# Performance work log

Measured on AMD Instinct MI355X. Metric: run time of the kernel, lower is better.

Reference implementation:

```python
import jax, jax.numpy as jnp
import numpy as np

N = 1024
IN_DIM = 64
H = 8
D = 8
E_REAL = 16384
GAMMA = 0.1


def setup_inputs() -> dict:
    key = jax.random.key(0)
    ks = jax.random.split(key, 12)
    inp = {
        "h": jax.random.normal(ks[0], (N, IN_DIM), dtype=jnp.float32),
        "e": jax.random.normal(ks[1], (E_REAL, IN_DIM), dtype=jnp.float32),
        "WQ": jax.random.normal(ks[2], (IN_DIM, H * D), dtype=jnp.float32) * 0.1,
        "WK": jax.random.normal(ks[3], (IN_DIM, H * D), dtype=jnp.float32) * 0.1,
        "WE": jax.random.normal(ks[4], (IN_DIM, H * D), dtype=jnp.float32) * 0.1,
        "WQ2": jax.random.normal(ks[5], (IN_DIM, H * D), dtype=jnp.float32) * 0.1,
        "WK2": jax.random.normal(ks[6], (IN_DIM, H * D), dtype=jnp.float32) * 0.1,
        "WE2": jax.random.normal(ks[7], (IN_DIM, H * D), dtype=jnp.float32) * 0.1,
        "WV": jax.random.normal(ks[8], (IN_DIM, H * D), dtype=jnp.float32) * 0.1,
        "real_src": jax.random.randint(ks[9], (E_REAL,), 0, N, dtype=jnp.int32),
        "real_dst": jax.random.randint(ks[10], (E_REAL,), 0, N, dtype=jnp.int32),
    }
    return inp


def reference(h, e, WQ, WK, WE, WQ2, WK2, WE2, WV, real_src, real_dst):
    scale = float(np.sqrt(D))
    # Dense edge-feature adjacency: adj[src, dst] = e  (zeros elsewhere)
    adj = jnp.zeros((N, N, IN_DIM), dtype=h.dtype).at[real_src, real_dst].set(e)
    # Edge projections over the dense adjacency (no bias): [N, N, H, D]
    Eh = (adj @ WE).reshape(N, N, H, D)
    E2h = (adj @ WE2).reshape(N, N, H, D)
    # Node projections: [N, H, D]
    Qh = (h @ WQ).reshape(N, H, D)
    Kh = (h @ WK).reshape(N, H, D)
    Q2h = (h @ WQ2).reshape(N, H, D)
    K2h = (h @ WK2).reshape(N, H, D)
    Vh = (h @ WV).reshape(N, H, D)
    # 3-way K*Q*E contraction over head dim: [N, N, H] (i = src, j = dst)
    weights_real = jnp.einsum('ihd,jhd,ijhd->ijh', Kh, Qh, Eh) / scale
    weights_fake = jnp.einsum('ihd,jhd,ijhd->ijh', K2h, Q2h, E2h) / scale
    weights_real_exp = jnp.exp(jnp.clip(weights_real, -5.0, 5.0)) / (GAMMA + 1.0)
    weights_fake_exp = GAMMA * jnp.exp(jnp.clip(weights_fake, -5.0, 5.0)) / (GAMMA + 1.0)
    # Blend: real-edge positions take the real attention value
    weights_final = weights_fake_exp.at[real_src, real_dst].set(
        weights_real_exp[real_src, real_dst])
    # Zero self-loops
    idx = jnp.arange(N)
    weights_final = weights_final.at[idx, idx].set(0.0)
    # Aggregate values at destination nodes: sum over src i -> [N, H, D]
    out = jnp.einsum('ijh,ihd->jhd', weights_final, Vh)
    # Normalizer: sum of attention weights per destination node [N, H, 1]
    z = jnp.sum(weights_final, axis=0).reshape(N, H, 1)
    return out / (z + 1e-6)
```

## Files before the change

### kernel.cpp

```cpp
#include <hip/hip_runtime.h>

#define NN     1024
#define INDIM  64
#define EREAL  16384
#define HD     64

__constant__ const float C_BASE    = 0.1f / 1.1f;
__constant__ const float INV_1P1   = 1.0f / 1.1f;
__constant__ const float INV_SCALE = 0.35355339059327373f;

__global__ void proj_kernel(const float* __restrict__ h,
                            const float* __restrict__ WQ,
                            const float* __restrict__ WK,
                            const float* __restrict__ WV,
                            float* __restrict__ Qh,
                            float* __restrict__ Kh,
                            float* __restrict__ Vh) {
    __shared__ float hrow[INDIM];
    const int row = blockIdx.x;
    const int t   = threadIdx.x;
    hrow[t] = h[row * INDIM + t];
    __syncthreads();
    float q = 0.f, k = 0.f, v = 0.f;
#pragma unroll 8
    for (int r = 0; r < INDIM; ++r) {
        const float hv = hrow[r];
        q += hv * WQ[r * HD + t];
        k += hv * WK[r * HD + t];
        v += hv * WV[r * HD + t];
    }
    Qh[row * HD + t] = q;
    Kh[row * HD + t] = k;
    Vh[row * HD + t] = v;
}

__global__ void colsum_kernel(const float* __restrict__ Vh, float* __restrict__ S) {
    __shared__ float part[4][HD];
    const int c = threadIdx.x & 63;
    const int p = threadIdx.x >> 6;
    float s = 0.f;
    for (int j = p * 256; j < p * 256 + 256; ++j) s += Vh[j * HD + c];
    part[p][c] = s;
    __syncthreads();
    if (p == 0) S[c] = part[0][c] + part[1][c] + part[2][c] + part[3][c];
}

__global__ void winner_kernel(const int* __restrict__ src, const int* __restrict__ dst,
                              int* __restrict__ winner) {
    const int k = blockIdx.x * 256 + threadIdx.x;
    if (k < EREAL) {
        const int key = src[k] * NN + dst[k];
        atomicMax(&winner[key], k + 1);
    }
}

__global__ void edge_kernel(const float* __restrict__ e,
                            const float* __restrict__ WE,
                            const float* __restrict__ Qh,
                            const float* __restrict__ Kh,
                            const float* __restrict__ Vh,
                            const int* __restrict__ src,
                            const int* __restrict__ dst,
                            const int* __restrict__ winner,
                            float* __restrict__ outacc,
                            float* __restrict__ zacc) {
    const int wid = threadIdx.x >> 6;
    const int k   = blockIdx.x * 4 + wid;
    const int t   = threadIdx.x & 63;
    const int s = src[k];
    const int d = dst[k];
    if (winner[s * NN + d] != k + 1 || s == d) return;

    const float ev = e[k * INDIM + t];
    float acc = 0.f;
#pragma unroll
    for (int r = 0; r < INDIM; ++r) {
        acc += __shfl(ev, r, 64) * WE[r * HD + t];
    }
    float term = Kh[s * HD + t] * Qh[d * HD + t] * acc;
    term += __shfl_xor(term, 1, 64);
    term += __shfl_xor(term, 2, 64);
    term += __shfl_xor(term, 4, 64);
    const float wr    = fminf(fmaxf(term * INV_SCALE, -5.f), 5.f);
    const float delta = expf(wr) * INV_1P1 - C_BASE;

    atomicAdd(&outacc[d * HD + t], delta * Vh[s * HD + t]);
    if ((t & 7) == 0) atomicAdd(&zacc[d * 8 + (t >> 3)], delta);
}

__global__ void finalize_kernel(const float* __restrict__ Vh,
                                const float* __restrict__ S,
                                const float* __restrict__ outacc,
                                const float* __restrict__ zacc,
                                float* __restrict__ out) {
    const int idx = blockIdx.x * 256 + threadIdx.x;
    const int j = idx >> 6;
    const int t = idx & 63;
    const float z = C_BASE * 1023.f + zacc[j * 8 + (t >> 3)] + 1e-6f;
    const float o = C_BASE * (S[t] - Vh[idx]) + outacc[idx];
    out[idx] = o / z;
}

extern "C" void kernel_launch(void* const* d_in, const int* in_sizes, int n_in,
                              void* d_out, int out_size, void* d_ws, size_t ws_size,
                              hipStream_t stream) {
    const float* h  = (const float*)d_in[0];
    const float* e  = (const float*)d_in[1];
    const float* WQ = (const float*)d_in[2];
    const float* WK = (const float*)d_in[3];
    const float* WE = (const float*)d_in[4];
    const float* WV = (const float*)d_in[8];
    const int* src  = (const int*)d_in[9];
    const int* dst  = (const int*)d_in[10];
    float* out = (float*)d_out;

    char* ws = (char*)d_ws;
    float* Qh = (float*)(ws + (0 << 10));
    float* Kh = (float*)(ws + (256 << 10));
    float* Vh = (float*)(ws + (512 << 10));
    float* S  = (float*)(ws + (768 << 10));
    char*  zreg   = ws + (1 << 20);
    float* outacc = (float*)zreg;
    float* zacc   = (float*)(zreg + (256 << 10));
    int*   winner = (int*)(zreg + (288 << 10));
    const size_t zbytes = (288 << 10) + (4u << 20);

    hipMemsetAsync(zreg, 0, zbytes, stream);
    hipLaunchKernelGGL(proj_kernel,    dim3(NN),   dim3(64),  0, stream, h, WQ, WK, WV, Qh, Kh, Vh);
    hipLaunchKernelGGL(colsum_kernel,  dim3(1),    dim3(256), 0, stream, Vh, S);
    hipLaunchKernelGGL(winner_kernel,  dim3(EREAL / 256), dim3(256), 0, stream, src, dst, winner);
    hipLaunchKernelGGL(edge_kernel,    dim3(EREAL / 4),   dim3(256), 0, stream,
                       e, WE, Qh, Kh, Vh, src, dst, winner, outacc, zacc);
    hipLaunchKernelGGL(finalize_kernel, dim3(NN * HD / 256), dim3(256), 0, stream,
                       Vh, S, outacc, zacc, out);
}
```

Measured before the change: 106.1 us.

## Fuse all stages into one cooperative kernel with grid syncs

Replaces the memset and five separate launches with a single cooperative kernel of 512 blocks. It runs projection, zeroing, winner resolution, column sums, edge processing and finalize as phases separated by grid.sync. The edge phase now has each wave handle 8 edges, broadcasting e values with readlane and reusing WE loads across them, and it uses the fast __expf. This removes launch gaps and the memset, at the cost of three grid-wide barriers and a fixed grid size tied to the problem dimensions.

Measured after the change: 279.2 us. +163.3%, slower.

```diff
diff --git a/kernel.cpp b/kernel.cpp
--- a/kernel.cpp
+++ b/kernel.cpp
@@ -1,104 +1,132 @@
 #include <hip/hip_runtime.h>
+#include <hip/hip_cooperative_groups.h>
+
+namespace cg = cooperative_groups;
 
 #define NN     1024
 #define INDIM  64
 #define EREAL  16384
 #define HD     64
+#define NBLK   512
+#define NTHR   256
 
-__constant__ const float C_BASE    = 0.1f / 1.1f;
-__constant__ const float INV_1P1   = 1.0f / 1.1f;
-__constant__ const float INV_SCALE = 0.35355339059327373f;
+constexpr float C_BASE    = 0.1f / 1.1f;
+constexpr float INV_1P1   = 1.0f / 1.1f;
+constexpr float INV_SCALE = 0.35355339059327373f;
 
-__global__ void proj_kernel(const float* __restrict__ h,
-                            const float* __restrict__ WQ,
-                            const float* __restrict__ WK,
-                            const float* __restrict__ WV,
-                            float* __restrict__ Qh,
-                            float* __restrict__ Kh,
-                            float* __restrict__ Vh) {
-    __shared__ float hrow[INDIM];
-    const int row = blockIdx.x;
-    const int t   = threadIdx.x;
-    hrow[t] = h[row * INDIM + t];
-    __syncthreads();
-    float q = 0.f, k = 0.f, v = 0.f;
-#pragma unroll 8
-    for (int r = 0; r < INDIM; ++r) {
-        const float hv = hrow[r];
-        q += hv * WQ[r * HD + t];
-        k += hv * WK[r * HD + t];
-        v += hv * WV[r * HD + t];
-    }
-    Qh[row * HD + t] = q;
-    Kh[row * HD + t] = k;
-    Vh[row * HD + t] = v;
+__device__ __forceinline__ float bcast(float v, int lane) {
+    return __uint_as_float(__builtin_amdgcn_readlane(__float_as_uint(v), lane));
 }
 
-__global__ void colsum_kernel(const float* __restrict__ Vh, float* __restrict__ S) {
-    __shared__ float part[4][HD];
-    const int c = threadIdx.x & 63;
-    const int p = threadIdx.x >> 6;
-    float s = 0.f;
-    for (int j = p * 256; j < p * 256 + 256; ++j) s += Vh[j * HD + c];
-    part[p][c] = s;
-    __syncthreads();
-    if (p == 0) S[c] = part[0][c] + part[1][c] + part[2][c] + part[3][c];
-}
+__global__ __launch_bounds__(NTHR, 2)
+void fused_kernel(const float* __restrict__ h,
+                  const float* __restrict__ e,
+                  const float* __restrict__ WQ,
+                  const float* __restrict__ WK,
+                  const float* __restrict__ WE,
+                  const float* __restrict__ WV,
+                  const int*   __restrict__ src,
+                  const int*   __restrict__ dst,
+                  float* __restrict__ Qh,
+                  float* __restrict__ Kh,
+                  float* __restrict__ Vh,
+                  float* __restrict__ outacc,
+                  float* __restrict__ zacc,
+                  float* __restrict__ Spart,
+                  int*   __restrict__ winner,
+                  float* __restrict__ out)
+{
+    cg::grid_group grid = cg::this_grid();
+    const int tid  = threadIdx.x;
+    const int bid  = blockIdx.x;
+    const int gtid = bid * NTHR + tid;
+    __shared__ float lds_buf[4][HD];
 
-__global__ void winner_kernel(const int* __restrict__ src, const int* __restrict__ dst,
-                              int* __restrict__ winner) {
-    const int k = blockIdx.x * 256 + threadIdx.x;
-    if (k < EREAL) {
-        const int key = src[k] * NN + dst[k];
-        atomicMax(&winner[key], k + 1);
+    if (bid >= 256) {
+        const int z = (bid - 256) * NTHR + tid;
+        const float4 zero4 = make_float4(0.f, 0.f, 0.f, 0.f);
+        float4* regA = (float4*)outacc;
+        if (z < 18688) regA[z] = zero4;
+        float4* regB = (float4*)winner;
+#pragma unroll
+        for (int i = 0; i < 4; ++i) regB[z + i * 65536] = zero4;
+    } else {
+        const int g = tid >> 6, c = tid & 63;
+        const int row = bid * 4 + g;
+        lds_buf[g][c] = h[row * INDIM + c];
+        __syncthreads();
+        float q = 0.f, k = 0.f, v = 0.f;
+#pragma unroll
+        for (int r = 0; r < INDIM; ++r) {
+            const float hv = lds_buf[g][r];
+            q = fmaf(hv, WQ[r * HD + c], q);
+            k = fmaf(hv, WK[r * HD + c], k);
+            v = fmaf(hv, WV[r * HD + c], v);
+        }
+        Qh[row * HD + c] = q;
+        Kh[row * HD + c] = k;
+        Vh[row * HD + c] = v;
     }
-}
+    grid.sync();
 
-__global__ void edge_kernel(const float* __restrict__ e,
-                            const float* __restrict__ WE,
-                            const float* __restrict__ Qh,
-                            const float* __restrict__ Kh,
-                            const float* __restrict__ Vh,
-                            const int* __restrict__ src,
-                            const int* __restrict__ dst,
-                            const int* __restrict__ winner,
-                            float* __restrict__ outacc,
-                            float* __restrict__ zacc) {
-    const int wid = threadIdx.x >> 6;
-    const int k   = blockIdx.x * 4 + wid;
-    const int t   = threadIdx.x & 63;
-    const int s = src[k];
-    const int d = dst[k];
-    if (winner[s * NN + d] != k + 1 || s == d) return;
+    if (gtid < EREAL) {
+        atomicMax(&winner[src[gtid] * NN + dst[gtid]], gtid + 1);
+    }
+    if (bid >= NBLK - 16) {
+        const int p = bid - (NBLK - 16);
+        const int g = tid >> 6, c = tid & 63;
+        float s = 0.f;
+        const int j0 = p * 64 + g * 16;
+        for (int j = j0; j < j0 + 16; ++j) s += Vh[j * HD + c];
+        lds_buf[g][c] = s;
+        __syncthreads();
+        if (g == 0)
+            Spart[p * HD + c] = lds_buf[0][c] + lds_buf[1][c] + lds_buf[2][c] + lds_buf[3][c];
+    }
+    grid.sync();
 
-    const float ev = e[k * INDIM + t];
-    float acc = 0.f;
+    {
+        const int wave = gtid >> 6;
+        const int t = tid & 63;
+        const int k0 = wave * 8;
+        float ev[8];
 #pragma unroll
-    for (int r = 0; r < INDIM; ++r) {
-        acc += __shfl(ev, r, 64) * WE[r * HD + t];
+        for (int i = 0; i < 8; ++i) ev[i] = e[(k0 + i) * INDIM + t];
+        float acc[8] = {0.f, 0.f, 0.f, 0.f, 0.f, 0.f, 0.f, 0.f};
+#pragma unroll
+        for (int r = 0; r < INDIM; ++r) {
+            const float w = WE[r * HD + t];
+#pragma unroll
+            for (int i = 0; i < 8; ++i)
+                acc[i] = fmaf(bcast(ev[i], r), w, acc[i]);
+        }
+#pragma unroll
+        for (int i = 0; i < 8; ++i) {
+            const int k = k0 + i;
+            const int s = src[k];
+            const int d = dst[k];
+            if (winner[s * NN + d] != k + 1 || s == d) continue;
+            float term = Kh[s * HD + t] * Qh[d * HD + t] * acc[i];
+            term += __shfl_xor(term, 1, 64);
+            term += __shfl_xor(term, 2, 64);
+            term += __shfl_xor(term, 4, 64);
+            const float wr    = fminf(fmaxf(term * INV_SCALE, -5.f), 5.f);
+            const float delta = __expf(wr) * INV_1P1 - C_BASE;
+            atomicAdd(&outacc[d * HD + t], delta * Vh[s * HD + t]);
+            if ((t & 7) == 0) atomicAdd(&zacc[d * 8 + (t >> 3)], delta);
+        }
     }
-    float term = Kh[s * HD + t] * Qh[d * HD + t] * acc;
-    term += __shfl_xor(term, 1, 64);
-    term += __shfl_xor(term, 2, 64);
-    term += __shfl_xor(term, 4, 64);
-    const float wr    = fminf(fmaxf(term * INV_SCALE, -5.f), 5.f);
-    const float delta = expf(wr) * INV_1P1 - C_BASE;
+    grid.sync();
 
-    atomicAdd(&outacc[d * HD + t], delta * Vh[s * HD + t]);
-    if ((t & 7) == 0) atomicAdd(&zacc[d * 8 + (t >> 3)], delta);
-}
-
-__global__ void finalize_kernel(const float* __restrict__ Vh,
-                                const float* __restrict__ S,
-                                const float* __restrict__ outacc,
-                                const float* __restrict__ zacc,
-                                float* __restrict__ out) {
-    const int idx = blockIdx.x * 256 + threadIdx.x;
-    const int j = idx >> 6;
-    const int t = idx & 63;
-    const float z = C_BASE * 1023.f + zacc[j * 8 + (t >> 3)] + 1e-6f;
-    const float o = C_BASE * (S[t] - Vh[idx]) + outacc[idx];
-    out[idx] = o / z;
+    if (bid < 256) {
+        const int idx = gtid;
+        const int j = idx >> 6, t = idx & 63;
+        float S = 0.f;
+#pragma unroll
+        for (int p = 0; p < 16; ++p) S += Spart[p * HD + t];
+        const float z = C_BASE * 1023.f + zacc[j * 8 + (t >> 3)] + 1e-6f;
+        out[idx] = fmaf(C_BASE, S - Vh[idx], outacc[idx]) / z;
+    }
 }
 
 extern "C" void kernel_launch(void* const* d_in, const int* in_sizes, int n_in,
@@ -115,22 +143,19 @@
     float* out = (float*)d_out;
 
     char* ws = (char*)d_ws;
-    float* Qh = (float*)(ws + (0 << 10));
-    float* Kh = (float*)(ws + (256 << 10));
-    float* Vh = (float*)(ws + (512 << 10));
-    float* S  = (float*)(ws + (768 << 10));
-    char*  zreg   = ws + (1 << 20);
-    float* outacc = (float*)zreg;
-    float* zacc   = (float*)(zreg + (256 << 10));
-    int*   winner = (int*)(zreg + (288 << 10));
-    const size_t zbytes = (288 << 10) + (4u << 20);
+    float* Qh     = (float*)(ws + (0    << 10));
+    float* Kh     = (float*)(ws + (256  << 10));
+    float* Vh     = (float*)(ws + (512  << 10));
+    float* outacc = (float*)(ws + (768  << 10));
+    float* zacc   = (float*)(ws + (1024 << 10));
+    float* Spart  = (float*)(ws + (1056 << 10));
+    int*   winner = (int*)  (ws + (2    << 20));
 
-    hipMemsetAsync(zreg, 0, zbytes, stream);
-    hipLaunchKernelGGL(proj_kernel,    dim3(NN),   dim3(64),  0, stream, h, WQ, WK, WV, Qh, Kh, Vh);
-    hipLaunchKernelGGL(colsum_kernel,  dim3(1),    dim3(256), 0, stream, Vh, S);
-    hipLaunchKernelGGL(winner_kernel,  dim3(EREAL / 256), dim3(256), 0, stream, src, dst, winner);
-    hipLaunchKernelGGL(edge_kernel,    dim3(EREAL / 4),   dim3(256), 0, stream,
-                       e, WE, Qh, Kh, Vh, src, dst, winner, outacc, zacc);
-    hipLaunchKernelGGL(finalize_kernel, dim3(NN * HD / 256), dim3(256), 0, stream,
-                       Vh, S, outacc, zacc, out);
+    void* args[] = {(void*)&h, (void*)&e, (void*)&WQ, (void*)&WK, (void*)&WE,
+                    (void*)&WV, (void*)&src, (void*)&dst,
+                    (void*)&Qh, (void*)&Kh, (void*)&Vh,
+                    (void*)&outacc, (void*)&zacc, (void*)&Spart,
+                    (void*)&winner, (void*)&out};
+    hipLaunchCooperativeKernel((const void*)fused_kernel, dim3(NBLK), dim3(NTHR),
+                               args, 0, stream);
 }
```
